# Optimization experiments

Measured on AMD Instinct MI355X. Metric: run time of the kernel, lower is better.

The kernel has to match this reference:

```python
import jax, jax.numpy as jnp
import numpy as np

N, NS, B = 4096, 256, 2
X, Y, Z = 128, 128, 16
R = 4                      # compress_ratio per spatial axis
C, NC, H = 128, 20, 8      # feat dim, num classes, heads
DH = C // H
EPS = 1e-5


def setup_inputs() -> dict:
    rng = np.random.default_rng(0)
    gx_n, gy_n, gz_n = X // R, Y // R, Z // R
    # pick NS//B unique super-voxel cells per batch element
    cells = np.stack([rng.choice(gx_n * gy_n * gz_n, NS // B, replace=False) for _ in range(B)])
    gx = cells // (gy_n * gz_n)
    rem = cells % (gy_n * gz_n)
    gy, gz = rem // gz_n, rem % gz_n
    bidx = np.repeat(np.arange(B), NS // B)
    sv = np.stack([bidx, gx.ravel(), gy.ravel(), gz.ravel()], axis=1)  # [NS,4]
    per = N // NS  # 16 voxels per super-voxel, distinct offsets in the 4x4x4 cell
    offs = np.argsort(rng.random((NS, R * R * R)), axis=1)[:, :per]
    dx, dy, dz = offs // (R * R), (offs // R) % R, offs % R
    vox = np.stack([
        np.repeat(sv[:, 0], per),
        (sv[:, 1, None] * R + dx).ravel(),
        (sv[:, 2, None] * R + dy).ravel(),
        (sv[:, 3, None] * R + dz).ravel()], axis=1).astype(np.int32)

    ks = jax.random.split(jax.random.key(0), 12)
    p = lambda k, shape, s=0.02: jax.random.normal(k, shape, jnp.float32) * s
    return dict(
        indices=jnp.asarray(vox),
        features=jax.random.normal(ks[0], (N, C), jnp.float32),
        cw1=p(ks[1], (C, C)), cb1=jnp.zeros(C), cg1=jnp.ones(C), cbe1=jnp.zeros(C),
        cw2=p(ks[2], (C, C)), cb2=jnp.zeros(C),
        pw1=p(ks[3], (3, 64)), pb1=jnp.zeros(64), pg1=jnp.ones(64), pbe1=jnp.zeros(64),
        pw2=p(ks[4], (64, 1)), pb2=jnp.zeros(1),
        wq=p(ks[5], (C, C)), bq=jnp.zeros(C),
        wk=p(ks[6], (C, C)), bk=jnp.zeros(C),
        wv=p(ks[7], (C, C)), bv=jnp.zeros(C),
        wo=p(ks[8], (C, C)), bo=jnp.zeros(C),
        ln_g=jnp.ones(C), ln_b=jnp.zeros(C),
        seg_w=p(ks[9], (3, 3, 3, C, NC)), seg_b=jnp.zeros(NC),
    )


def _bn(x, g, b):  # BatchNorm1d, training-mode batch statistics
    mu = x.mean(0)
    var = x.var(0)
    return (x - mu) * jax.lax.rsqrt(var + EPS) * g + b


def reference(indices, features, cw1, cb1, cg1, cbe1, cw2, cb2,
              pw1, pb1, pg1, pbe1, pw2, pb2,
              wq, bq, wk, bk, wv, bv, wo, bo, ln_g, ln_b, seg_w, seg_b):
    ratio = jnp.array([1, R, R, R], dtype=indices.dtype)
    comp = indices // ratio                                  # [N,4] super-voxel coord
    unq, inv = jnp.unique(comp, axis=0, size=NS, return_inverse=True)
    # scatter-add softmax(features) over super-voxels
    cf = jax.ops.segment_sum(jax.nn.softmax(features, axis=1), inv, num_segments=NS)
    h = jax.nn.relu(_bn(cf @ cw1 + cb1, cg1, cbe1)) @ cw2 + cb2      # [NS,C]
    # pairwise relative-position bias: tiny MLP over [N*NS,3]
    pos = (indices[:, None, 1:] - unq[None, :, 1:]).astype(jnp.float32).reshape(N * NS, 3)
    pbias = (jax.nn.relu(_bn(pos @ pw1 + pb1, pg1, pbe1)) @ pw2 + pb2).reshape(N, NS)
    # multi-head cross attention: voxels query super-voxels, bias added to scores
    q = (features @ wq + bq).reshape(N, H, DH)
    k = (h @ wk + bk).reshape(NS, H, DH)
    v = (h @ wv + bv).reshape(NS, H, DH)
    scores = jnp.einsum('nhd,shd->hns', q, k) / np.float32(np.sqrt(DH)) + pbias[None]
    attn = jax.nn.softmax(scores, axis=-1)                   # [H,N,NS]
    ctx = jnp.einsum('hns,shd->nhd', attn, v).reshape(N, C) @ wo + bo
    y = features + ctx                                       # residual + LayerNorm sublayer
    mu = y.mean(-1, keepdims=True)
    var = y.var(-1, keepdims=True)
    y = (y - mu) * jax.lax.rsqrt(var + EPS) * ln_g + ln_b
    # SubMConv3d(128->20, k=3, pad=1): dense scatter -> conv -> gather at active sites
    grid = jnp.zeros((B, X, Y, Z, C), jnp.float32).at[
        indices[:, 0], indices[:, 1], indices[:, 2], indices[:, 3]].set(y)
    out = jax.lax.conv_general_dilated(
        grid, seg_w, (1, 1, 1), 'SAME',
        dimension_numbers=('NDHWC', 'DHWIO', 'NDHWC')) + seg_b
    return out[indices[:, 0], indices[:, 1], indices[:, 2], indices[:, 3]]  # [N,NC]
```

## Files before the change

kernel.cpp:

```cpp
#include <hip/hip_runtime.h>

typedef unsigned short ushort_t;

#define NVOX 4096
#define NSV  256
#define XD   128
#define YD   128
#define ZD   16
#define CD   128
#define NCD  20
#define HD   8
#define DHD  16
#define MAPN 524288
#define EPSF 1e-5f

#define OF_FEAT 0
#define OF_CW1  524288
#define OF_CB1  540672
#define OF_CG1  540800
#define OF_CBE1 540928
#define OF_CW2  541056
#define OF_CB2  557440
#define OF_PW1  557568
#define OF_PB1  557760
#define OF_PG1  557824
#define OF_PBE1 557888
#define OF_PW2  557952
#define OF_PB2  558016
#define OF_WQ   558080
#define OF_BQ   574464
#define OF_WK   574592
#define OF_BK   590976
#define OF_WV   591104
#define OF_BV   607488
#define OF_WO   607616
#define OF_BO   624000
#define OF_LNG  624128
#define OF_LNB  624256
#define OF_SEGW 624384
#define OF_SEGB 693504
#define ARENA_N 693568
#define TOTCVT  624341

__device__ __forceinline__ float bf2f(const ushort_t* p){
  return __uint_as_float(((unsigned)(*p)) << 16);
}
__device__ __forceinline__ ushort_t f2bf(float f){
  unsigned u = __float_as_uint(f);
  u += 0x7fffu + ((u >> 16) & 1u);
  return (ushort_t)(u >> 16);
}
__device__ __forceinline__ float unlo(unsigned u){ return __uint_as_float(u << 16); }
__device__ __forceinline__ float unhi(unsigned u){ return __uint_as_float(u & 0xffff0000u); }

struct SrcPtrs { const void* p[25]; };

__device__ const int g_cnt[25] = {524288,16384,128,128,128,16384,128,192,64,64,64,64,1,
                                  16384,128,16384,128,16384,128,16384,128,128,128,0,20};
__device__ const int g_off[25] = {OF_FEAT,OF_CW1,OF_CB1,OF_CG1,OF_CBE1,OF_CW2,OF_CB2,
                                  OF_PW1,OF_PB1,OF_PG1,OF_PBE1,OF_PW2,OF_PB2,
                                  OF_WQ,OF_BQ,OF_WK,OF_BK,OF_WV,OF_BV,OF_WO,OF_BO,
                                  OF_LNG,OF_LNB,OF_SEGW,OF_SEGB};

__device__ __forceinline__ float ldi(const void* p, int off, int fl){
  return fl ? bf2f((const ushort_t*)p + off) : ((const float*)p)[off];
}

struct SPREP {
  float frows[16][CD];
  float qpart[2][16][CD];
  float part[8][CD];
  float cfs[CD];
  float gpart[8][CD];
};
union __align__(16) UPREP { SPREP sv; int smom[18]; };

__global__ __launch_bounds__(512) void kprep(SrcPtrs sp, const int* idx, int* flag,
    float* arena, float* wt, int* map, float* afold_g, float* scfold_g,
    float* qb, float* t1T)
{
  __shared__ UPREP sm;
  __shared__ int sm_flag;
  int t = threadIdx.x, b = blockIdx.x;
  if (t < 64){
    const ushort_t* f16 = (const ushort_t*)sp.p[0];
    unsigned u = f16[2*t];
    int e = (u >> 7) & 0xFF;
    int sane = (u == 0 || (e >= 90 && e <= 150)) ? 1 : 0;
    unsigned long long bl = __ballot(sane);
    if (t == 0) sm_flag = (__popcll(bl) >= 48) ? 1 : 0;
  }
  __syncthreads();
  const int fl = sm_flag;

  if (b < 255){
    int gid = b*512 + t;
    const int GS = 255*512;
    if (gid == 0) *flag = fl;
    for (int k=gid; k<MAPN; k+=GS) map[k] = -1;
    for (int el=gid; el<TOTCVT; el+=GS){
      int s=0, rem=el;
      while (rem >= g_cnt[s]){ rem -= g_cnt[s]; ++s; }
      arena[g_off[s]+rem] = ldi(sp.p[s], rem, fl);
    }
    for (int k=gid; k<27*NCD*CD; k+=GS){
      int nb = k/(NCD*CD); int rem = k - nb*(NCD*CD); int o = rem/CD, i = rem - o*CD;
      wt[k] = ldi(sp.p[23], nb*(CD*NCD) + i*NCD + o, fl);
    }
  } else if (b < 511){
    int sv = b - 255;
    int rb = sv*16;
    if (fl){
      const uint2* fsrc = (const uint2*)((const ushort_t*)sp.p[0] + (size_t)rb*CD);
      uint2 u = fsrc[t];
      float* dst = &sm.sv.frows[t>>5][(t&31)*4];
      dst[0]=unlo(u.x); dst[1]=unhi(u.x); dst[2]=unlo(u.y); dst[3]=unhi(u.y);
    } else {
      const float4* fsrc = (const float4*)((const float*)sp.p[0] + (size_t)rb*CD);
      ((float4*)sm.sv.frows)[t] = fsrc[t];
    }
    __syncthreads();
    {
      int c8 = (t&15)*8, r = (t>>4)&15, kh = t>>8;
      int i0 = kh*64;
      float acc[8] = {0.f,0.f,0.f,0.f,0.f,0.f,0.f,0.f};
      if (fl){
        const ushort_t* wqp = (const ushort_t*)sp.p[13];
        #pragma unroll 4
        for (int i=i0; i<i0+64; ++i){
          uint4 w4 = *(const uint4*)(wqp + (size_t)i*CD + c8);
          float fr = sm.sv.frows[r][i];
          acc[0] += unlo(w4.x)*fr; acc[1] += unhi(w4.x)*fr;
          acc[2] += unlo(w4.y)*fr; acc[3] += unhi(w4.y)*fr;
          acc[4] += unlo(w4.z)*fr; acc[5] += unhi(w4.z)*fr;
          acc[6] += unlo(w4.w)*fr; acc[7] += unhi(w4.w)*fr;
        }
      } else {
        const float* wqp = (const float*)sp.p[13];
        #pragma unroll 4
        for (int i=i0; i<i0+64; ++i){
          float4 wa = *(const float4*)(wqp + (size_t)i*CD + c8);
          float4 wb = *(const float4*)(wqp + (size_t)i*CD + c8 + 4);
          float fr = sm.sv.frows[r][i];
          acc[0]+=wa.x*fr; acc[1]+=wa.y*fr; acc[2]+=wa.z*fr; acc[3]+=wa.w*fr;
          acc[4]+=wb.x*fr; acc[5]+=wb.y*fr; acc[6]+=wb.z*fr; acc[7]+=wb.w*fr;
        }
      }
      #pragma unroll
      for (int j=0;j<8;++j) sm.sv.qpart[kh][r][c8+j] = acc[j];
    }
    __syncthreads();
    for (int e = t; e < 16*CD; e += 512){
      int r = e>>7, c = e&127;
      qb[(size_t)(rb+r)*CD + c] = sm.sv.qpart[0][r][c] + sm.sv.qpart[1][r][c]
                                + ldi(sp.p[14], c, fl);
    }
    {
      int w = t>>6, l = t&63;
      float a0 = 0.f, a1 = 0.f;
      #pragma unroll
      for (int k=0;k<2;++k){
        int r = w*2 + k;
        float f0 = sm.sv.frows[r][l];
        float f1 = sm.sv.frows[r][l+64];
        float m = fmaxf(f0,f1);
        #pragma unroll
        for (int o=32;o;o>>=1) m = fmaxf(m, __shfl_xor(m,o,64));
        float e0 = __expf(f0-m), e1 = __expf(f1-m);
        float ssum = e0+e1;
        #pragma unroll
        for (int o=32;o;o>>=1) ssum += __shfl_xor(ssum,o,64);
        float inv = 1.f/ssum;
        a0 += e0*inv; a1 += e1*inv;
      }
      sm.sv.part[w][l] = a0; sm.sv.part[w][l+64] = a1;
    }
    __syncthreads();
    if (t < CD){
      float s = 0.f;
      #pragma unroll
      for (int w=0;w<8;++w) s += sm.sv.part[w][t];
      sm.sv.cfs[t] = s;
    }
    __syncthreads();
    {
      int c2 = (t&63)*2, kg = t>>6;
      int i0 = kg*16;
      float a0 = 0.f, a1 = 0.f;
      if (fl){
        const ushort_t* W = (const ushort_t*)sp.p[1];
        #pragma unroll 4
        for (int i=i0; i<i0+16; ++i){
          unsigned w = *(const unsigned*)(W + (size_t)i*CD + c2);
          float cfv = sm.sv.cfs[i];
          a0 += unlo(w)*cfv; a1 += unhi(w)*cfv;
        }
      } else {
        const float* W = (const float*)sp.p[1];
        #pragma unroll 4
        for (int i=i0; i<i0+16; ++i){
          float2 w = *(const float2*)(W + (size_t)i*CD + c2);
          float cfv = sm.sv.cfs[i];
          a0 += w.x*cfv; a1 += w.y*cfv;
        }
      }
      sm.sv.gpart[kg][c2] = a0; sm.sv.gpart[kg][c2+1] = a1;
    }
    __syncthreads();
    if (t < CD){
      float s = 0.f;
      #pragma unroll
      for (int kg=0;kg<8;++kg) s += sm.sv.gpart[kg][t];
      t1T[(size_t)t*NSV + sv] = s + ldi(sp.p[2], t, fl);
    }
  } else {
    if (t < 18) sm.smom[t] = 0;
    __syncthreads();
    {
      int sacc[9] = {0,0,0,0,0,0,0,0,0};
      for (int v = t; v < NVOX; v += 512){
        int4 q = ((const int4*)idx)[v];
        sacc[0]+=q.y; sacc[1]+=q.z; sacc[2]+=q.w;
        sacc[3]+=q.y*q.y; sacc[4]+=q.z*q.z; sacc[5]+=q.w*q.w;
        sacc[6]+=q.y*q.z; sacc[7]+=q.y*q.w; sacc[8]+=q.z*q.w;
      }
      int um[9] = {0,0,0,0,0,0,0,0,0};
      if (t < 256){
        int4 q = ((const int4*)idx)[t*16];
        int gx=q.y>>2, gy=q.z>>2, gz=q.w>>2;
        um[0]=gx; um[1]=gy; um[2]=gz;
        um[3]=gx*gx; um[4]=gy*gy; um[5]=gz*gz;
        um[6]=gx*gy; um[7]=gx*gz; um[8]=gy*gz;
      }
      int lane = t & 63;
      #pragma unroll
      for (int i=0;i<9;++i){
        int s = sacc[i];
        int u = um[i];
        #pragma unroll
        for (int o=32;o;o>>=1){
          s += __shfl_xor(s, o, 64);
          u += __shfl_xor(u, o, 64);
        }
        if (lane == 0){
          if (s) atomicAdd(&sm.smom[9+i], s);
          if (u) atomicAdd(&sm.smom[i], u);
        }
      }
    }
    __syncthreads();
    if (t < 64){
      int* smom = sm.smom;
      double U1[3]={(double)smom[0],(double)smom[1],(double)smom[2]};
      double S1[3]={(double)smom[9],(double)smom[10],(double)smom[11]};
      double Uxx[3][3], Sxx[3][3];
      Uxx[0][0]=smom[3]; Uxx[1][1]=smom[4]; Uxx[2][2]=smom[5];
      Uxx[0][1]=Uxx[1][0]=smom[6]; Uxx[0][2]=Uxx[2][0]=smom[7]; Uxx[1][2]=Uxx[2][1]=smom[8];
      Sxx[0][0]=smom[12]; Sxx[1][1]=smom[13]; Sxx[2][2]=smom[14];
      Sxx[0][1]=Sxx[1][0]=smom[15]; Sxx[0][2]=Sxx[2][0]=smom[16]; Sxx[1][2]=Sxx[2][1]=smom[17];
      double M1[3], M2[3][3];
      for (int a=0;a<3;++a) M1[a] = 256.0*S1[a] - 4096.0*U1[a];
      for (int a=0;a<3;++a)
        for (int b2=0;b2<3;++b2)
          M2[a][b2] = 256.0*Sxx[a][b2] - S1[a]*U1[b2] - S1[b2]*U1[a] + 4096.0*Uxx[a][b2];
      double wv_[3]={(double)ldi(sp.p[7],t,fl),(double)ldi(sp.p[7],64+t,fl),(double)ldi(sp.p[7],128+t,fl)};
      double bj=(double)ldi(sp.p[8],t,fl), gj=(double)ldi(sp.p[9],t,fl), bej=(double)ldi(sp.p[10],t,fl);
      double Mw=0.0, wMw=0.0;
      for (int a=0;a<3;++a){
        Mw += M1[a]*wv_[a];
        for (int b2=0;b2<3;++b2) wMw += wv_[a]*M2[a][b2]*wv_[b2];
      }
      const double NM = 1048576.0;
      double mean = Mw/NM + bj;
      double Ey2  = wMw/NM + 2.0*bj*Mw/NM + bj*bj;
      double var  = Ey2 - mean*mean;
      double scale = gj / sqrt(var + 1e-5);
      afold_g[t]      = (float)(wv_[0]*scale);
      afold_g[64+t]   = (float)(wv_[1]*scale);
      afold_g[128+t]  = (float)(wv_[2]*scale);
      scfold_g[t]     = (float)(bj*scale + bej - mean*scale);
    }
  }
}

__global__ __launch_bounds__(256) void k6_fused(const float* t1T, const float* A,
    const int* idx, int* map, float* kb, float* vb){
  __shared__ float row[CD];
  __shared__ float cpar[2][CD];
  __shared__ float hrow[CD];
  int t = threadIdx.x;
  int role = blockIdx.x >> 8, s = blockIdx.x & 255;
  if (role == 0 && t >= 128 && t < 144){
    int v = s*16 + (t-128);
    int4 q = ((const int4*)idx)[v];
    map[((q.x*XD + q.y)*YD + q.z)*ZD + q.w] = v;
  }
  if (t < CD){
    const float4* col = (const float4*)(t1T + (size_t)t*NSV);
    float sum=0.f, sq=0.f;
    #pragma unroll 8
    for (int i=0;i<NSV/4;++i){
      float4 v = col[i];
      sum += v.x+v.y+v.z+v.w;
      sq  += v.x*v.x+v.y*v.y+v.z*v.z+v.w*v.w;
    }
    float mean = sum*(1.f/256.f);
    float var  = sq*(1.f/256.f) - mean*mean;
    float scv = A[OF_CG1+t]*rsqrtf(var+EPSF);
    float shv = A[OF_CBE1+t] - mean*scv;
    row[t] = fmaxf(t1T[(size_t)t*NSV + s]*scv + shv, 0.f);
  }
  __syncthreads();
  int c = t&127, half = t>>7;
  {
    const float* W = A + OF_CW2;
    float acc = 0.f;
    #pragma unroll 8
    for (int i=half*64;i<half*64+64;++i) acc += row[i]*W[i*CD+c];
    cpar[half][c] = acc;
  }
  __syncthreads();
  if (t < CD) hrow[t] = cpar[0][t]+cpar[1][t]+A[OF_CB2+t];
  __syncthreads();
  {
    const float* W = role ? (A+OF_WV) : (A+OF_WK);
    float acc = 0.f;
    #pragma unroll 8
    for (int i=half*64;i<half*64+64;++i) acc += hrow[i]*W[i*CD+c];
    cpar[half][c] = acc;
  }
  __syncthreads();
  if (t < CD){
    float v = cpar[0][t]+cpar[1][t] + (role ? A[OF_BV+t] : A[OF_BK+t]);
    if (role) vb[(size_t)s*CD+t] = v; else kb[(size_t)s*CD+t] = v;
  }
}

__global__ __launch_bounds__(256) void k9_attn(
    const float* A, const int* idx, const float* afold_g, const float* scfold_g,
    const float* kb, const float* vb, const float* qb, float* yb)
{
  __shared__ __align__(16) float q4s[4][CD];
  __shared__ __align__(16) float scf[NSV][36];
  __shared__ __align__(16) float ctxT[CD*4];
  __shared__ float cpart[2][4][CD];
  __shared__ __align__(16) float e4T[64][4];
  __shared__ float saf[3][64];
  __shared__ float ssc[64];
  __shared__ float w2s[64];
  __shared__ float rinv[32];
  int t = threadIdx.x;
  int n0 = blockIdx.x*4;
  if (t < 128) ((float4*)q4s)[t] = ((const float4*)(qb + (size_t)n0*CD))[t];
  if (t < 64){
    saf[0][t] = afold_g[t]; saf[1][t] = afold_g[64+t]; saf[2][t] = afold_g[128+t];
    ssc[t] = scfold_g[t]; w2s[t] = A[OF_PW2+t];
  }
  __syncthreads();
  {
    int g = t>>6, j = t&63;
    float xv = (float)idx[4*(n0+g)+1];
    float yv = (float)idx[4*(n0+g)+2];
    float zv = (float)idx[4*(n0+g)+3];
    e4T[j][g] = saf[0][j]*xv + saf[1][j]*yv + saf[2][j]*zv;
  }
  __syncthreads();
  {
    int4 q0 = ((const int4*)idx)[t*16];
    float uxf = (float)(q0.y>>2), uyf = (float)(q0.z>>2), uzf = (float)(q0.w>>2);
    float pbv[4];
    float pb2v = A[OF_PB2];
    #pragma unroll
    for (int g=0;g<4;++g) pbv[g] = pb2v;
    #pragma unroll 2
    for (int j=0;j<64;++j){
      float dj = ssc[j] - (saf[0][j]*uxf + saf[1][j]*uyf + saf[2][j]*uzf);
      float wj = w2s[j];
      float4 ea = *(const float4*)&e4T[j][0];
      pbv[0] += fmaxf(ea.x+dj,0.f)*wj; pbv[1] += fmaxf(ea.y+dj,0.f)*wj;
      pbv[2] += fmaxf(ea.z+dj,0.f)*wj; pbv[3] += fmaxf(ea.w+dj,0.f)*wj;
    }
    const float4* krow = (const float4*)(kb + (size_t)t*CD);
    float4 kc0 = krow[0], kc1 = krow[1], kc2 = krow[2], kc3 = krow[3];
    for (int h=0;h<HD;++h){
      int hn = (h+1)&7;
      float4 kn0 = krow[hn*4+0], kn1 = krow[hn*4+1];
      float4 kn2 = krow[hn*4+2], kn3 = krow[hn*4+3];
      float p[4];
      #pragma unroll
      for (int g=0;g<4;++g){
        const float* qg = &q4s[g][h*DHD];
        float dot = qg[0]*kc0.x + qg[1]*kc0.y + qg[2]*kc0.z + qg[3]*kc0.w
                  + qg[4]*kc1.x + qg[5]*kc1.y + qg[6]*kc1.z + qg[7]*kc1.w
                  + qg[8]*kc2.x + qg[9]*kc2.y + qg[10]*kc2.z + qg[11]*kc2.w
                  + qg[12]*kc3.x + qg[13]*kc3.y + qg[14]*kc3.z + qg[15]*kc3.w;
        p[g] = __expf(dot*0.25f + pbv[g]);
      }
      *(float4*)&scf[t][h*4] = make_float4(p[0],p[1],p[2],p[3]);
      kc0 = kn0; kc1 = kn1; kc2 = kn2; kc3 = kn3;
    }
  }
  __syncthreads();
  {
    int g = t>>6, lane = t&63;
    for (int h=0;h<HD;++h){
      int col = h*4 + g;
      float s0 = scf[lane][col] + scf[lane+64][col] + scf[lane+128][col] + scf[lane+192][col];
      #pragma unroll
      for (int o=32;o;o>>=1) s0 += __shfl_xor(s0,o,64);
      if (lane==0) rinv[g*8+h] = 1.f/s0;
    }
  }
  __syncthreads();
  {
    int half=t>>7, c=t&127, h=c>>4;
    const float* vcol = vb + c;
    float acc[4]={0.f,0.f,0.f,0.f};
    #pragma unroll 4
    for (int s0=half*128; s0<half*128+128; s0+=4){
      float v0=vcol[(s0+0)*CD], v1=vcol[(s0+1)*CD], v2=vcol[(s0+2)*CD], v3=vcol[(s0+3)*CD];
      float4 p0 = *(const float4*)&scf[s0+0][h*4];
      float4 p1 = *(const float4*)&scf[s0+1][h*4];
      float4 p2 = *(const float4*)&scf[s0+2][h*4];
      float4 p3 = *(const float4*)&scf[s0+3][h*4];
      acc[0] += p0.x*v0 + p1.x*v1 + p2.x*v2 + p3.x*v3;
      acc[1] += p0.y*v0 + p1.y*v1 + p2.y*v2 + p3.y*v3;
      acc[2] += p0.z*v0 + p1.z*v1 + p2.z*v2 + p3.z*v3;
      acc[3] += p0.w*v0 + p1.w*v1 + p2.w*v2 + p3.w*v3;
    }
    #pragma unroll
    for (int g=0;g<4;++g) cpart[half][g][c]=acc[g];
  }
  __syncthreads();
  if (t < CD){
    int h = t>>4;
    #pragma unroll
    for (int g=0;g<4;++g)
      ctxT[t*4+g] = (cpart[0][g][t]+cpart[1][g][t])*rinv[g*8+h];
  }
  __syncthreads();
  {
    int half=t>>7, c=t&127;
    const float* wo = A + OF_WO;
    float acc[4]={0.f,0.f,0.f,0.f};
    #pragma unroll 4
    for (int i=half*64;i<half*64+64;++i){
      float wv = wo[i*CD+c];
      float4 r = *(const float4*)&ctxT[i*4];
      acc[0]+=r.x*wv; acc[1]+=r.y*wv; acc[2]+=r.z*wv; acc[3]+=r.w*wv;
    }
    #pragma unroll
    for (int g=0;g<4;++g) cpart[half][g][c]=acc[g];
  }
  __syncthreads();
  if (t < CD){
    float bov = A[OF_BO+t];
    #pragma unroll
    for (int g=0;g<4;++g)
      ctxT[t*4+g] = cpart[0][g][t]+cpart[1][g][t] + bov
                  + A[OF_FEAT + (size_t)(n0+g)*CD + t];
  }
  __syncthreads();
  {
    int g = t>>6, lane = t&63;
    float x0 = ctxT[lane*4+g], x1 = ctxT[(lane+64)*4+g];
    float s1 = x0+x1, s2 = x0*x0+x1*x1;
    #pragma unroll
    for (int o=32;o;o>>=1){ s1 += __shfl_xor(s1,o,64); s2 += __shfl_xor(s2,o,64); }
    float mean = s1*(1.f/128.f);
    float var  = s2*(1.f/128.f) - mean*mean;
    float rs = rsqrtf(var + EPSF);
    yb[(size_t)(n0+g)*CD + lane]    = (x0-mean)*rs*A[OF_LNG+lane]    + A[OF_LNB+lane];
    yb[(size_t)(n0+g)*CD + lane+64] = (x1-mean)*rs*A[OF_LNG+lane+64] + A[OF_LNB+lane+64];
  }
}

__global__ __launch_bounds__(256) void k10_conv(const int* idx, const int* map,
    const float* yb, const float* A, const float* wt, const int* flag, void* outv)
{
  __shared__ int sco4[8][4];
  __shared__ int jn[8][27];
  __shared__ float partial[4][8][NCD];
  int t = threadIdx.x;
  int p0 = blockIdx.x*8;
  if (t < 32) ((int*)sco4)[t] = idx[4*p0 + t];
  __syncthreads();
  if (t < 216){
    int v = t/27, nb = t - v*27;
    int kd = nb/9, kh = (nb/3)%3, kw = nb%3;
    int bb = sco4[v][0];
    int nx = sco4[v][1]+kd-1, ny = sco4[v][2]+kh-1, nz = sco4[v][3]+kw-1;
    int j = -1;
    if ((unsigned)nx < XD && (unsigned)ny < YD && (unsigned)nz < ZD)
      j = map[((bb*XD+nx)*YD+ny)*ZD+nz];
    jn[v][nb] = j;
  }
  __syncthreads();
  int w = t>>6, l = t&63;
  int og = l & 3, cg = l >> 2;
  int c0 = cg*8;
  float acc[8][5];
  #pragma unroll
  for (int v=0;v<8;++v)
    #pragma unroll
    for (int oo=0;oo<5;++oo) acc[v][oo]=0.f;
  for (int nb = w; nb < 27; nb += 4){
    const float* wbase = wt + (size_t)nb*NCD*CD + c0;
    float4 wreg[10];
    #pragma unroll
    for (int oo=0;oo<5;++oo){
      wreg[oo*2]   = *(const float4*)(wbase + (size_t)(og*5+oo)*CD);
      wreg[oo*2+1] = *(const float4*)(wbase + (size_t)(og*5+oo)*CD + 4);
    }
    #pragma unroll
    for (int v=0; v<8; ++v){
      int j = jn[v][nb];
      if (j < 0) continue;
      const float4* y4 = (const float4*)(yb + (size_t)j*CD + c0);
      float4 ya = y4[0], ybb = y4[1];
      #pragma unroll
      for (int oo=0;oo<5;++oo){
        float4 wa = wreg[oo*2], wb = wreg[oo*2+1];
        acc[v][oo] += ya.x*wa.x + ya.y*wa.y + ya.z*wa.z + ya.w*wa.w
                    + ybb.x*wb.x + ybb.y*wb.y + ybb.z*wb.z + ybb.w*wb.w;
      }
    }
  }
  #pragma unroll
  for (int v=0;v<8;++v)
    #pragma unroll
    for (int oo=0;oo<5;++oo){
      float s = acc[v][oo];
      s += __shfl_xor(s, 4, 64);
      s += __shfl_xor(s, 8, 64);
      s += __shfl_xor(s, 16, 64);
      s += __shfl_xor(s, 32, 64);
      if (cg == 0) partial[w][v][og*5+oo] = s;
    }
  __syncthreads();
  if (t < 160){
    int v = t/20, o = t - v*20;
    float s = partial[0][v][o]+partial[1][v][o]+partial[2][v][o]+partial[3][v][o]
            + A[OF_SEGB+o];
    if (*flag) ((ushort_t*)outv)[(size_t)(p0+v)*NCD + o] = f2bf(s);
    else       ((float*)outv)[(size_t)(p0+v)*NCD + o]   = s;
  }
}

extern "C" void kernel_launch(void* const* d_in, const int* in_sizes, int n_in,
                              void* d_out, int out_size, void* d_ws, size_t ws_size,
                              hipStream_t stream) {
  const int* idx = (const int*)d_in[0];

  char* w = (char*)d_ws;
  size_t off = 0;
  #define ALLOC(name, type, count) \
    type* name = (type*)(w + off); off += (((size_t)(count)*sizeof(type)) + 255) & ~(size_t)255;
  ALLOC(flag,   int,   64)
  ALLOC(arena,  float, ARENA_N)
  ALLOC(wt,     float, 27*NCD*CD)
  ALLOC(map,    int,   MAPN)
  ALLOC(afold,  float, 192)
  ALLOC(scfold, float, 64)
  ALLOC(t1T,    float, CD*NSV)
  ALLOC(kb,     float, NSV*CD)
  ALLOC(vbuf,   float, NSV*CD)
  ALLOC(qb,     float, NVOX*CD)
  ALLOC(yb,     float, NVOX*CD)
  #undef ALLOC
  (void)off; (void)ws_size; (void)n_in; (void)in_sizes; (void)out_size;

  SrcPtrs sp;
  for (int i=0;i<25;++i) sp.p[i] = d_in[i+1];

  kprep   <<<512, 512, 0, stream>>>(sp, idx, flag, arena, wt, map, afold, scfold, qb, t1T);
  k6_fused<<<NSV*2, 256, 0, stream>>>(t1T, arena, idx, map, kb, vbuf);
  k9_attn <<<NVOX/4, 256, 0, stream>>>(arena, idx, afold, scfold, kb, vbuf, qb, yb);
  k10_conv<<<NVOX/8, 256, 0, stream>>>(idx, map, yb, arena, wt, flag, d_out);
}
```

Baseline: 207.7 us.

## Split attention heads into two passes to shrink score buffer and raise occupancy

The attention kernel now handles the 8 heads in two passes of 4, so the shared score buffer per block drops from 36 to 16 floats per super-voxel row. Each pass does its own normalisation reduction and V accumulation, with the V loop split four ways over super-voxels. A rotating column swizzle on the score buffer is meant to cut shared-memory bank conflicts, and launch bounds now request 6 blocks per CU so the lower LDS use can turn into higher occupancy. In exchange the kernel gains extra barriers and drops the previous software prefetch of K rows.

```diff
diff --git a/kernel.cpp b/kernel.cpp
--- a/kernel.cpp
+++ b/kernel.cpp
@@ -336,14 +336,16 @@
   }
 }
 
-__global__ __launch_bounds__(256) void k9_attn(
+#define CGRP(row,hh) (((hh) + ((row)>>1)) & 3)
+
+__global__ __launch_bounds__(256, 6) void k9_attn(
     const float* A, const int* idx, const float* afold_g, const float* scfold_g,
     const float* kb, const float* vb, const float* qb, float* yb)
 {
   __shared__ __align__(16) float q4s[4][CD];
-  __shared__ __align__(16) float scf[NSV][36];
+  __shared__ __align__(16) float scf[NSV][16];
   __shared__ __align__(16) float ctxT[CD*4];
-  __shared__ float cpart[2][4][CD];
+  __shared__ float cpart[4][4][64];
   __shared__ __align__(16) float e4T[64][4];
   __shared__ float saf[3][64];
   __shared__ float ssc[64];
@@ -365,10 +367,10 @@
     e4T[j][g] = saf[0][j]*xv + saf[1][j]*yv + saf[2][j]*zv;
   }
   __syncthreads();
+  float pbv[4];
   {
     int4 q0 = ((const int4*)idx)[t*16];
     float uxf = (float)(q0.y>>2), uyf = (float)(q0.z>>2), uzf = (float)(q0.w>>2);
-    float pbv[4];
     float pb2v = A[OF_PB2];
     #pragma unroll
     for (int g=0;g<4;++g) pbv[g] = pb2v;
@@ -380,63 +382,64 @@
       pbv[0] += fmaxf(ea.x+dj,0.f)*wj; pbv[1] += fmaxf(ea.y+dj,0.f)*wj;
       pbv[2] += fmaxf(ea.z+dj,0.f)*wj; pbv[3] += fmaxf(ea.w+dj,0.f)*wj;
     }
-    const float4* krow = (const float4*)(kb + (size_t)t*CD);
-    float4 kc0 = krow[0], kc1 = krow[1], kc2 = krow[2], kc3 = krow[3];
-    for (int h=0;h<HD;++h){
-      int hn = (h+1)&7;
-      float4 kn0 = krow[hn*4+0], kn1 = krow[hn*4+1];
-      float4 kn2 = krow[hn*4+2], kn3 = krow[hn*4+3];
-      float p[4];
-      #pragma unroll
-      for (int g=0;g<4;++g){
-        const float* qg = &q4s[g][h*DHD];
-        float dot = qg[0]*kc0.x + qg[1]*kc0.y + qg[2]*kc0.z + qg[3]*kc0.w
-                  + qg[4]*kc1.x + qg[5]*kc1.y + qg[6]*kc1.z + qg[7]*kc1.w
-                  + qg[8]*kc2.x + qg[9]*kc2.y + qg[10]*kc2.z + qg[11]*kc2.w
-                  + qg[12]*kc3.x + qg[13]*kc3.y + qg[14]*kc3.z + qg[15]*kc3.w;
-        p[g] = __expf(dot*0.25f + pbv[g]);
-      }
-      *(float4*)&scf[t][h*4] = make_float4(p[0],p[1],p[2],p[3]);
-      kc0 = kn0; kc1 = kn1; kc2 = kn2; kc3 = kn3;
-    }
-  }
-  __syncthreads();
-  {
-    int g = t>>6, lane = t&63;
-    for (int h=0;h<HD;++h){
-      int col = h*4 + g;
-      float s0 = scf[lane][col] + scf[lane+64][col] + scf[lane+128][col] + scf[lane+192][col];
-      #pragma unroll
-      for (int o=32;o;o>>=1) s0 += __shfl_xor(s0,o,64);
-      if (lane==0) rinv[g*8+h] = 1.f/s0;
-    }
-  }
-  __syncthreads();
-  {
-    int half=t>>7, c=t&127, h=c>>4;
-    const float* vcol = vb + c;
-    float acc[4]={0.f,0.f,0.f,0.f};
-    #pragma unroll 4
-    for (int s0=half*128; s0<half*128+128; s0+=4){
-      float v0=vcol[(s0+0)*CD], v1=vcol[(s0+1)*CD], v2=vcol[(s0+2)*CD], v3=vcol[(s0+3)*CD];
-      float4 p0 = *(const float4*)&scf[s0+0][h*4];
-      float4 p1 = *(const float4*)&scf[s0+1][h*4];
-      float4 p2 = *(const float4*)&scf[s0+2][h*4];
-      float4 p3 = *(const float4*)&scf[s0+3][h*4];
-      acc[0] += p0.x*v0 + p1.x*v1 + p2.x*v2 + p3.x*v3;
-      acc[1] += p0.y*v0 + p1.y*v1 + p2.y*v2 + p3.y*v3;
-      acc[2] += p0.z*v0 + p1.z*v1 + p2.z*v2 + p3.z*v3;
-      acc[3] += p0.w*v0 + p1.w*v1 + p2.w*v2 + p3.w*v3;
-    }
-    #pragma unroll
-    for (int g=0;g<4;++g) cpart[half][g][c]=acc[g];
-  }
-  __syncthreads();
-  if (t < CD){
-    int h = t>>4;
-    #pragma unroll
-    for (int g=0;g<4;++g)
-      ctxT[t*4+g] = (cpart[0][g][t]+cpart[1][g][t])*rinv[g*8+h];
+  }
+  const float4* krow = (const float4*)(kb + (size_t)t*CD);
+  #pragma unroll
+  for (int p=0;p<2;++p){
+    {
+      #pragma unroll
+      for (int hh=0; hh<4; ++hh){
+        int h = p*4 + hh;
+        float4 k0 = krow[h*4+0], k1 = krow[h*4+1], k2 = krow[h*4+2], k3 = krow[h*4+3];
+        float pr[4];
+        #pragma unroll
+        for (int g=0; g<4; ++g){
+          const float* qg = &q4s[g][h*DHD];
+          float dot = qg[0]*k0.x + qg[1]*k0.y + qg[2]*k0.z + qg[3]*k0.w
+                    + qg[4]*k1.x + qg[5]*k1.y + qg[6]*k1.z + qg[7]*k1.w
+                    + qg[8]*k2.x + qg[9]*k2.y + qg[10]*k2.z + qg[11]*k2.w
+                    + qg[12]*k3.x + qg[13]*k3.y + qg[14]*k3.z + qg[15]*k3.w;
+          pr[g] = __expf(dot*0.25f + pbv[g]);
+        }
+        *(float4*)&scf[t][CGRP(t,hh)*4] = make_float4(pr[0],pr[1],pr[2],pr[3]);
+      }
+    }
+    __syncthreads();
+    {
+      int g = t>>6, lane = t&63;
+      #pragma unroll
+      for (int hh=0; hh<4; ++hh){
+        float s0 = 0.f;
+        #pragma unroll
+        for (int k=0;k<4;++k){
+          int r = lane + 64*k;
+          s0 += scf[r][CGRP(r,hh)*4 + g];
+        }
+        #pragma unroll
+        for (int o=32;o;o>>=1) s0 += __shfl_xor(s0,o,64);
+        if (lane==0) rinv[g*8 + p*4 + hh] = 1.f/s0;
+      }
+    }
+    {
+      int q = t>>6, c = t&63;
+      int hh = c>>4;
+      const float* vcol = vb + p*64 + c;
+      float a0=0.f, a1=0.f, a2=0.f, a3=0.f;
+      #pragma unroll 4
+      for (int s=q*64; s<q*64+64; ++s){
+        float v = vcol[(size_t)s*CD];
+        float4 pv = *(const float4*)&scf[s][CGRP(s,hh)*4];
+        a0 += pv.x*v; a1 += pv.y*v; a2 += pv.z*v; a3 += pv.w*v;
+      }
+      cpart[q][0][c]=a0; cpart[q][1][c]=a1; cpart[q][2][c]=a2; cpart[q][3][c]=a3;
+    }
+    __syncthreads();
+    {
+      int gsel = t>>6, c = t&63;
+      int ch = p*64 + c, h = ch>>4;
+      ctxT[ch*4+gsel] = (cpart[0][gsel][c]+cpart[1][gsel][c]
+                        +cpart[2][gsel][c]+cpart[3][gsel][c]) * rinv[gsel*8+h];
+    }
   }
   __syncthreads();
   {
@@ -450,14 +453,15 @@
       acc[0]+=r.x*wv; acc[1]+=r.y*wv; acc[2]+=r.z*wv; acc[3]+=r.w*wv;
     }
     #pragma unroll
-    for (int g=0;g<4;++g) cpart[half][g][c]=acc[g];
+    for (int g=0;g<4;++g) cpart[(c>>6)*2 + half][g][c&63] = acc[g];
   }
   __syncthreads();
   if (t < CD){
     float bov = A[OF_BO+t];
+    int chi = t>>6, cl = t&63;
     #pragma unroll
     for (int g=0;g<4;++g)
-      ctxT[t*4+g] = cpart[0][g][t]+cpart[1][g][t] + bov
+      ctxT[t*4+g] = cpart[chi*2+0][g][cl] + cpart[chi*2+1][g][cl] + bov
                   + A[OF_FEAT + (size_t)(n0+g)*CD + t];
   }
   __syncthreads();
```

New measurement: 204.6 us. Within noise of the previous version (-1.5%).
